# Performance work log

Measured on AMD Instinct MI355X. Metric: run time of the kernel, lower is better.

The kernel has to match this reference:

```python
import jax, jax.numpy as jnp
import numpy as np

E, DM, DH, K, DIL = 8, 512, 1024, 3, 2
N, L = 128, 128
PAD = DIL * (K - 1) // 2  # 'same' padding


def _conv1d(x, w):
    # x: [N, Cin, L], w: [Cout, Cin, K] -> [N, Cout, L]
    return jax.lax.conv_general_dilated(
        x, w, window_strides=(1,), padding=[(PAD, PAD)],
        rhs_dilation=(DIL,), dimension_numbers=("NCH", "OIH", "NCH"))


def _moe_conv(x, W, B, onehot):
    # W: [E, Cout, Cin, K], B: [E, Cout], onehot: [N, E]
    ys = jax.vmap(lambda w, b: _conv1d(x, w) + b[None, :, None])(W, B)  # [E, N, Cout, L]
    return jnp.einsum("enol,ne->nol", ys, onehot)


def setup_inputs() -> dict:
    key = jax.random.key(0)
    k1, k2, k3, k4, k5 = jax.random.split(key, 5)
    inp = jax.random.normal(k1, (N, DM, L), dtype=jnp.float32)
    # uneven per-expert sample counts summing to N (samples pre-sorted by expert)
    fwd_expert_count = jnp.asarray(np.array([10, 20, 16, 16, 12, 22, 14, 18], dtype=np.int32))
    w1 = jax.random.normal(k2, (E, DH, DM, K), dtype=jnp.float32) * 0.02
    b1 = jax.random.normal(k3, (E, DH), dtype=jnp.float32) * 0.02
    w2 = jax.random.normal(k4, (E, DM, DH, K), dtype=jnp.float32) * 0.02
    b2 = jax.random.normal(k5, (E, DM), dtype=jnp.float32) * 0.02
    return {"inp": inp, "fwd_expert_count": fwd_expert_count,
            "w1": w1, "b1": b1, "w2": w2, "b2": b2}


def reference(inp, fwd_expert_count, w1, b1, w2, b2):
    # map each sample index to its expert via cumulative counts
    cs = jnp.cumsum(fwd_expert_count)
    eid = jnp.searchsorted(cs, jnp.arange(N), side="right")  # [N]
    onehot = (eid[:, None] == jnp.arange(E)[None, :]).astype(inp.dtype)  # [N, E]
    h = _moe_conv(inp, w1, b1, onehot)       # [N, DH, L]
    h = jax.nn.gelu(h)
    out = _moe_conv(h, w2, b2, onehot)       # [N, DM, L]
    return out
```

## Files before the change

### kernel.cpp

```cpp
#include <hip/hip_runtime.h>
#include <hip/hip_bf16.h>
#include <stdint.h>


typedef __attribute__((ext_vector_type(8))) short short8;
typedef __attribute__((ext_vector_type(4))) float f32x4;

#define DMV 512
#define DHV 1024

#define OFF_X   0ull
#define OFF_H   (16ull << 20)
#define OFF_W1  (48ull << 20)
#define OFF_W2  (72ull << 20)

#define VMW(n) asm volatile("s_waitcnt vmcnt(" #n ")" ::: "memory")
#define SB __builtin_amdgcn_sched_barrier(0)

__device__ __forceinline__ uint16_t f2bf(float f) {
  uint32_t u = __builtin_bit_cast(uint32_t, f);
  uint32_t r = (u + 0x7FFFu + ((u >> 16) & 1u)) >> 16;
  return (uint16_t)r;
}

__device__ __forceinline__ void async_copy16(const void* g, void* l) {
  __builtin_amdgcn_global_load_lds(
      (const __attribute__((address_space(1))) uint32_t*)g,
      (__attribute__((address_space(3))) uint32_t*)l, 16, 0, 0);
}

__device__ __forceinline__ float gelu_f(float x) {
  float u = 0.7978845608028654f * (x + 0.044715f * x * x * x);
  float t = __expf(2.0f * u);
  float th = 1.0f - 2.0f / (t + 1.0f);
  return 0.5f * x * (1.0f + th);
}

__global__ __launch_bounds__(256) void prep_x_t(const float* __restrict__ inp,
                                                uint16_t* __restrict__ xp) {
  uint32_t b = blockIdx.x;
  uint32_t s = b >> 4, cc = b & 15u;
  __shared__ uint16_t xs[32][132];
  uint32_t t = threadIdx.x;
  const float* src0 = inp + ((size_t)s * DMV + cc * 32u) * 128u;
#pragma unroll
  for (int i = 0; i < 4; ++i) {
    uint32_t idx = (uint32_t)i * 256u + t;
    uint32_t ch = idx >> 5, l4 = idx & 31u;
    float4 f = *(const float4*)(src0 + ch * 128u + l4 * 4u);
    uint2 pk;
    pk.x = (uint32_t)f2bf(f.x) | ((uint32_t)f2bf(f.y) << 16);
    pk.y = (uint32_t)f2bf(f.z) | ((uint32_t)f2bf(f.w) << 16);
    *(uint2*)&xs[ch][l4 * 4u] = pk;
  }
  __syncthreads();
  uint32_t l = t >> 1, half = t & 1u;
  uint32_t fl = ((l + 2u) >> 1) & 3u;
#pragma unroll
  for (int hi = 0; hi < 2; ++hi) {
    uint32_t sub = half * 2u + (uint32_t)hi;
    uint32_t cg = (sub ^ fl) & 3u;
    uint32_t pk[4];
#pragma unroll
    for (int p2 = 0; p2 < 4; ++p2) {
      uint32_t c0 = cg * 8u + (uint32_t)p2 * 2u;
      pk[p2] = (uint32_t)xs[c0][l] | ((uint32_t)xs[c0 + 1][l] << 16);
    }
    uint4 v; v.x = pk[0]; v.y = pk[1]; v.z = pk[2]; v.w = pk[3];
    size_t slot = (((size_t)s * 16u + cc) * 128u + l) * 4u + sub;
    *(uint4*)(xp + slot * 8u) = v;
  }
}

template <int LOGCG, int LOGO>
__global__ __launch_bounds__(256) void prep_w_c(const float* __restrict__ w,
                                                uint16_t* __restrict__ wp) {
  constexpr uint32_t C = 4u << LOGCG;
  constexpr uint32_t CCn = C >> 5;
  constexpr uint32_t MTn = 1u << (LOGO - 7);
  uint32_t t = blockIdx.x * 256u + threadIdx.x;
  uint32_t cg = t & ((1u << LOGCG) - 1u);
  uint32_t o = (t >> LOGCG) & ((1u << LOGO) - 1u);
  uint32_t e = t >> (LOGCG + LOGO);
  uint32_t row = o & 127u, mt = o >> 7;
  const float* src = w + (((size_t)(e << LOGO) + o) * C + cg * 4u) * 3u;
  float4 f0 = *(const float4*)(src);
  float4 f1 = *(const float4*)(src + 4);
  float4 f2 = *(const float4*)(src + 8);
  uint32_t cc = cg >> 3;
  uint32_t sub = (cg >> 1) & 3u;
  uint32_t j0 = (cg & 1u) * 4u;
  size_t base = (((size_t)e * CCn + cc) * MTn + mt) * 3u;
  uint2 q;
  q.x = (uint32_t)f2bf(f0.x) | ((uint32_t)f2bf(f0.w) << 16);
  q.y = (uint32_t)f2bf(f1.z) | ((uint32_t)f2bf(f2.y) << 16);
  *(uint2*)(wp + ((base + 0u) * 128u + row) * 32u + sub * 8u + j0) = q;
  q.x = (uint32_t)f2bf(f0.y) | ((uint32_t)f2bf(f1.x) << 16);
  q.y = (uint32_t)f2bf(f1.w) | ((uint32_t)f2bf(f2.z) << 16);
  *(uint2*)(wp + ((base + 1u) * 128u + row) * 32u + sub * 8u + j0) = q;
  q.x = (uint32_t)f2bf(f0.z) | ((uint32_t)f2bf(f1.y) << 16);
  q.y = (uint32_t)f2bf(f2.x) | ((uint32_t)f2bf(f2.w) << 16);
  *(uint2*)(wp + ((base + 2u) * 128u + row) * 32u + sub * 8u + j0) = q;
}

template <int PHASE>
__global__ __launch_bounds__(PHASE == 1 ? 256 : 128, 2) void conv_mfma(
    const uint16_t* __restrict__ bprep, const uint16_t* __restrict__ wprep,
    const float* __restrict__ bias, const int* __restrict__ cnt,
    uint16_t* __restrict__ hout, float* __restrict__ fout) {
  constexpr int CC  = (PHASE == 1) ? 16 : 32;
  constexpr int MTP = (PHASE == 1) ? 8 : 4;
  constexpr int NW  = (PHASE == 1) ? 4 : 2;
  constexpr int NT  = NW * 64;
  constexpr int SLD = 8 / NW;
  constexpr int OO  = (PHASE == 1) ? DHV : DMV;

  uint32_t b = blockIdx.x;
  uint32_t xcd = b & 7u, i = b >> 3;
  const int s = (int)((xcd & 1u) * 64u + i);
  const int mt = (int)(xcd >> 1);
  const int mtBase = (PHASE == 1) ? mt * 2 : mt;
  int e = 0;
  { int cum = cnt[0]; while (s >= cum && e < 7) { ++e; cum += cnt[e]; } }
  const int tid = threadIdx.x;
  const int lane = tid & 63;
  const int wv = tid >> 6;
  const int l15 = lane & 15, kg = lane >> 4;

  __shared__ __align__(16) uint8_t lds[2 * 8448];

  const size_t AST = (size_t)MTP * 12288;
  const uint16_t* wLane = wprep + ((size_t)e * CC * MTP + mtBase) * 12288
                          + (uint32_t)(l15 * 32 + kg * 8);
  const uint16_t* xBase = bprep + (size_t)s * CC * 4096;

  if (tid < 32) {
    uint32_t n = (uint32_t)tid >> 4, ri = ((uint32_t)tid >> 2) & 3u, sb = (uint32_t)tid & 3u;
    uint32_t rowByte = (ri < 2) ? ri * 64u : (8320u + (ri - 2) * 64u);
    uint4 z = make_uint4(0, 0, 0, 0);
    *(uint4*)(lds + n * 8448u + rowByte + sb * 16u) = z;
  }

  {
    uint8_t* bw = lds + 128u;
#pragma unroll
    for (int t = 0; t < SLD; ++t)
      async_copy16(xBase + (t * NT + tid) * 8, bw + (uint32_t)(t * NT + tid) * 16);
  }
  SB;
  short8 aA[3][4], aB[3][4];
#pragma unroll
  for (int k = 0; k < 3; ++k)
#pragma unroll
    for (int q = 0; q < 4; ++q) {
      uint32_t rows = (uint32_t)(wv * 64 + q * 16);
      aA[k][q] = *(const short8*)(wLane + (rows >> 7) * 12288u +
                                  ((uint32_t)k * 128u + (rows & 127u)) * 32u);
    }
  VMW(0);
  asm volatile("s_waitcnt lgkmcnt(0)" ::: "memory");
  __builtin_amdgcn_s_barrier();

  f32x4 acc[4][8] = {};

  auto STEP = [&](short8 (&CUR)[3][4], short8 (&NXT)[3][4], int cc, bool pre) {
    const uint8_t* bb = lds + (uint32_t)(cc & 1) * 8448u;
    if (pre) {
      const uint16_t* xs = xBase + (size_t)(cc + 1) * 4096;
      uint8_t* bw = lds + (uint32_t)((cc + 1) & 1) * 8448u + 128u;
#pragma unroll
      for (int t = 0; t < SLD; ++t)
        async_copy16(xs + (t * NT + tid) * 8, bw + (uint32_t)(t * NT + tid) * 16);
      SB;
    }
    const uint16_t* aP = wLane + (size_t)(cc + 1) * AST;
#pragma unroll
    for (int k = 0; k < 3; ++k) {
      if (pre) {
#pragma unroll
        for (int q = 0; q < 4; ++q) {
          uint32_t rows = (uint32_t)(wv * 64 + q * 16);
          NXT[k][q] = *(const short8*)(aP + (rows >> 7) * 12288u +
                                       ((uint32_t)k * 128u + (rows & 127u)) * 32u);
        }
      }
      short8 bf[8];
#pragma unroll
      for (int bq = 0; bq < 8; ++bq) {
        uint32_t r = (uint32_t)(bq * 16 + l15 + 2 * k);
        bf[bq] = *(const short8*)(bb + r * 64u +
                                  (((uint32_t)kg ^ (r >> 1)) & 3u) * 16u);
      }
      __builtin_amdgcn_s_setprio(1);
#pragma unroll
      for (int q = 0; q < 4; ++q)
#pragma unroll
        for (int bq = 0; bq < 8; ++bq)
          acc[q][bq] = __builtin_amdgcn_mfma_f32_16x16x32_bf16(
              CUR[k][q], bf[bq], acc[q][bq], 0, 0, 0);
      __builtin_amdgcn_s_setprio(0);
    }
    if (pre) {
      VMW(12);
      __builtin_amdgcn_s_barrier();
    }
  };

#pragma unroll 1
  for (int cc = 0; cc < CC - 2; cc += 2) {
    STEP(aA, aB, cc, true);
    STEP(aB, aA, cc + 1, true);
  }
  STEP(aA, aB, CC - 2, true);
  STEP(aB, aA, CC - 1, false);

  if (PHASE == 1) {
#pragma unroll
    for (int a = 0; a < 4; ++a) {
      int ob = mt * 256 + wv * 64 + a * 16 + kg * 4;
      float4 bv = *(const float4*)(bias + (size_t)e * OO + ob);
      int cc2 = mt * 8 + wv * 2 + (a >> 1);
      uint32_t g = (uint32_t)((a & 1) * 2 + (kg >> 1));
      uint32_t j0 = (uint32_t)((kg & 1) * 4);
#pragma unroll
      for (int bq = 0; bq < 8; ++bq) {
        int l = bq * 16 + l15;
        uint32_t flq = ((uint32_t)(l + 2) >> 1) & 3u;
        uint32_t sub = g ^ flq;
        float v0 = gelu_f(acc[a][bq][0] + bv.x);
        float v1 = gelu_f(acc[a][bq][1] + bv.y);
        float v2 = gelu_f(acc[a][bq][2] + bv.z);
        float v3 = gelu_f(acc[a][bq][3] + bv.w);
        uint2 pk;
        pk.x = (uint32_t)f2bf(v0) | ((uint32_t)f2bf(v1) << 16);
        pk.y = (uint32_t)f2bf(v2) | ((uint32_t)f2bf(v3) << 16);
        size_t ci = ((size_t)s * 32 + cc2) * 128 + l;
        *(uint2*)(hout + ci * 32 + sub * 8 + j0) = pk;
      }
    }
  } else {
#pragma unroll
    for (int a = 0; a < 4; ++a) {
      int ob = mt * 128 + wv * 64 + a * 16 + kg * 4;
      float4 bv = *(const float4*)(bias + (size_t)e * OO + ob);
      float bvr[4] = {bv.x, bv.y, bv.z, bv.w};
      float* op = fout + ((size_t)s * DMV + ob) * 128;
#pragma unroll
      for (int bq = 0; bq < 8; ++bq) {
        int l = bq * 16 + l15;
#pragma unroll
        for (int r = 0; r < 4; ++r)
          op[(size_t)r * 128 + l] = acc[a][bq][r] + bvr[r];
      }
    }
  }
}

extern "C" void kernel_launch(void* const* d_in, const int* in_sizes, int n_in,
                              void* d_out, int out_size, void* d_ws, size_t ws_size,
                              hipStream_t stream) {
  const float* inp = (const float*)d_in[0];
  const int* cnt = (const int*)d_in[1];
  const float* w1 = (const float*)d_in[2];
  const float* b1 = (const float*)d_in[3];
  const float* w2 = (const float*)d_in[4];
  const float* b2 = (const float*)d_in[5];
  float* out = (float*)d_out;
  uint8_t* ws = (uint8_t*)d_ws;
  uint16_t* xp = (uint16_t*)(ws + OFF_X);
  uint16_t* hp = (uint16_t*)(ws + OFF_H);
  uint16_t* w1p = (uint16_t*)(ws + OFF_W1);
  uint16_t* w2p = (uint16_t*)(ws + OFF_W2);

  prep_x_t<<<dim3(2048), dim3(256), 0, stream>>>(inp, xp);
  prep_w_c<7, 10><<<dim3(4096), dim3(256), 0, stream>>>(w1, w1p);
  prep_w_c<8, 9><<<dim3(4096), dim3(256), 0, stream>>>(w2, w2p);
  conv_mfma<1><<<dim3(512), dim3(256), 0, stream>>>(xp, w1p, b1, cnt, hp, nullptr);
  conv_mfma<2><<<dim3(512), dim3(128), 0, stream>>>(hp, w2p, b2, cnt, nullptr, out);
}
```

Before: 164.2 us.

## Stage conv weights through swizzled LDS and shrink phase-1 blocks to two waves

Weights are now staged into LDS with async copies, using a swizzled layout written by the prep kernel. Previously each lane loaded its weight fragments straight from global memory into registers. Halo zero rows in LDS are replaced by clamped addresses plus register zeroing at the edges. Phase 1 now runs 1024 blocks of 128 threads instead of 512 of 256, and the block mapping changes. The aim is fewer uncoalesced global loads and lower register pressure, at the cost of an extra barrier and a full wait per channel chunk, with less overlap than the old double-buffered register prefetch.

New measurement: 170.5 us. 3.8% more time.

```diff
diff --git a/kernel.cpp b/kernel.cpp
--- a/kernel.cpp
+++ b/kernel.cpp
@@ -88,7 +88,7 @@
   float4 f1 = *(const float4*)(src + 4);
   float4 f2 = *(const float4*)(src + 8);
   uint32_t cc = cg >> 3;
-  uint32_t sub = (cg >> 1) & 3u;
+  uint32_t sub = ((cg >> 1) & 3u) ^ ((row >> 1) & 3u);
   uint32_t j0 = (cg & 1u) * 4u;
   size_t base = (((size_t)e * CCn + cc) * MTn + mt) * 3u;
   uint2 q;
@@ -104,122 +104,109 @@
 }
 
 template <int PHASE>
-__global__ __launch_bounds__(PHASE == 1 ? 256 : 128, 2) void conv_mfma(
+__global__ __launch_bounds__(128, 2) void conv_mfma(
     const uint16_t* __restrict__ bprep, const uint16_t* __restrict__ wprep,
     const float* __restrict__ bias, const int* __restrict__ cnt,
     uint16_t* __restrict__ hout, float* __restrict__ fout) {
   constexpr int CC  = (PHASE == 1) ? 16 : 32;
   constexpr int MTP = (PHASE == 1) ? 8 : 4;
-  constexpr int NW  = (PHASE == 1) ? 4 : 2;
-  constexpr int NT  = NW * 64;
-  constexpr int SLD = 8 / NW;
   constexpr int OO  = (PHASE == 1) ? DHV : DMV;
 
   uint32_t b = blockIdx.x;
-  uint32_t xcd = b & 7u, i = b >> 3;
-  const int s = (int)((xcd & 1u) * 64u + i);
-  const int mt = (int)(xcd >> 1);
-  const int mtBase = (PHASE == 1) ? mt * 2 : mt;
+  int s, mt;
+  if (PHASE == 1) { mt = (int)(b & 7u); s = (int)(b >> 3); }
+  else { uint32_t x = b & 7u; mt = (int)(x >> 1); s = (int)((x & 1u) * 64u + (b >> 3)); }
   int e = 0;
   { int cum = cnt[0]; while (s >= cum && e < 7) { ++e; cum += cnt[e]; } }
   const int tid = threadIdx.x;
   const int lane = tid & 63;
-  const int wv = tid >> 6;
+  const int mg = tid >> 6;
   const int l15 = lane & 15, kg = lane >> 4;
 
-  __shared__ __align__(16) uint8_t lds[2 * 8448];
-
-  const size_t AST = (size_t)MTP * 12288;
-  const uint16_t* wLane = wprep + ((size_t)e * CC * MTP + mtBase) * 12288
-                          + (uint32_t)(l15 * 32 + kg * 8);
+  __shared__ __align__(16) uint8_t lds[40960];
+
+  uint32_t aOff[4];
+#pragma unroll
+  for (int a = 0; a < 4; ++a) {
+    uint32_t ri = (uint32_t)(mg * 64 + a * 16 + l15);
+    aOff[a] = ri * 64u + (((uint32_t)kg ^ (ri >> 1)) & 3u) * 16u;
+  }
+  uint32_t bOff[3][8];
+#pragma unroll
+  for (int k = 0; k < 3; ++k)
+#pragma unroll
+    for (int bq = 0; bq < 8; ++bq) {
+      int r = l15 + bq * 16 + 2 * k - 2;
+      uint32_t rc = (uint32_t)(r < 0 ? 0 : (r > 127 ? 127 : r));
+      bOff[k][bq] = rc * 64u + (((uint32_t)kg ^ (((rc + 2u) >> 1))) & 3u) * 16u;
+    }
+  const bool zLow = (l15 < 2);
+  const bool zHigh = (l15 >= 14);
+
+  const uint16_t* wBase = wprep + ((size_t)e * CC * MTP + mt) * 12288;
   const uint16_t* xBase = bprep + (size_t)s * CC * 4096;
 
-  if (tid < 32) {
-    uint32_t n = (uint32_t)tid >> 4, ri = ((uint32_t)tid >> 2) & 3u, sb = (uint32_t)tid & 3u;
-    uint32_t rowByte = (ri < 2) ? ri * 64u : (8320u + (ri - 2) * 64u);
-    uint4 z = make_uint4(0, 0, 0, 0);
-    *(uint4*)(lds + n * 8448u + rowByte + sb * 16u) = z;
-  }
-
-  {
-    uint8_t* bw = lds + 128u;
-#pragma unroll
-    for (int t = 0; t < SLD; ++t)
-      async_copy16(xBase + (t * NT + tid) * 8, bw + (uint32_t)(t * NT + tid) * 16);
-  }
-  SB;
-  short8 aA[3][4], aB[3][4];
-#pragma unroll
-  for (int k = 0; k < 3; ++k)
-#pragma unroll
-    for (int q = 0; q < 4; ++q) {
-      uint32_t rows = (uint32_t)(wv * 64 + q * 16);
-      aA[k][q] = *(const short8*)(wLane + (rows >> 7) * 12288u +
-                                  ((uint32_t)k * 128u + (rows & 127u)) * 32u);
-    }
+  auto STAGE_A = [&](int cc) {
+    const uint16_t* src = wBase + (size_t)cc * (MTP * 12288);
+#pragma unroll
+    for (int i = 0; i < 12; ++i)
+      async_copy16(src + (i * 128 + tid) * 8, lds + (uint32_t)(i * 128 + tid) * 16u);
+  };
+  auto STAGE_B = [&](int cc) {
+    const uint16_t* src = xBase + (size_t)cc * 4096;
+    uint8_t* dst = lds + 24576u + (uint32_t)(cc & 1) * 8192u;
+#pragma unroll
+    for (int i = 0; i < 4; ++i)
+      async_copy16(src + (i * 128 + tid) * 8, dst + (uint32_t)(i * 128 + tid) * 16u);
+  };
+
+  STAGE_A(0); STAGE_B(0);
   VMW(0);
-  asm volatile("s_waitcnt lgkmcnt(0)" ::: "memory");
   __builtin_amdgcn_s_barrier();
 
   f32x4 acc[4][8] = {};
-
-  auto STEP = [&](short8 (&CUR)[3][4], short8 (&NXT)[3][4], int cc, bool pre) {
-    const uint8_t* bb = lds + (uint32_t)(cc & 1) * 8448u;
-    if (pre) {
-      const uint16_t* xs = xBase + (size_t)(cc + 1) * 4096;
-      uint8_t* bw = lds + (uint32_t)((cc + 1) & 1) * 8448u + 128u;
-#pragma unroll
-      for (int t = 0; t < SLD; ++t)
-        async_copy16(xs + (t * NT + tid) * 8, bw + (uint32_t)(t * NT + tid) * 16);
-      SB;
-    }
-    const uint16_t* aP = wLane + (size_t)(cc + 1) * AST;
+  const short8 z8 = {};
+
+#pragma unroll 1
+  for (int cc = 0; cc < CC; ++cc) {
+    short8 af[3][4];
+#pragma unroll
+    for (int k = 0; k < 3; ++k)
+#pragma unroll
+      for (int q = 0; q < 4; ++q)
+        af[k][q] = *(const short8*)(lds + (uint32_t)(k * 8192) + aOff[q]);
+    asm volatile("s_waitcnt lgkmcnt(0)" ::: "memory");
+    SB;
+    __builtin_amdgcn_s_barrier();
+    if (cc + 1 < CC) { STAGE_A(cc + 1); STAGE_B(cc + 1); }
+    const uint8_t* bb = lds + 24576u + (uint32_t)(cc & 1) * 8192u;
 #pragma unroll
     for (int k = 0; k < 3; ++k) {
-      if (pre) {
-#pragma unroll
-        for (int q = 0; q < 4; ++q) {
-          uint32_t rows = (uint32_t)(wv * 64 + q * 16);
-          NXT[k][q] = *(const short8*)(aP + (rows >> 7) * 12288u +
-                                       ((uint32_t)k * 128u + (rows & 127u)) * 32u);
-        }
+      __builtin_amdgcn_s_setprio(1);
+#pragma unroll
+      for (int bq = 0; bq < 8; ++bq) {
+        short8 bf = *(const short8*)(bb + bOff[k][bq]);
+        if (k == 0 && bq == 0) bf = zLow ? z8 : bf;
+        if (k == 2 && bq == 7) bf = zHigh ? z8 : bf;
+#pragma unroll
+        for (int q = 0; q < 4; ++q)
+          acc[q][bq] = __builtin_amdgcn_mfma_f32_16x16x32_bf16(
+              af[k][q], bf, acc[q][bq], 0, 0, 0);
       }
-      short8 bf[8];
-#pragma unroll
-      for (int bq = 0; bq < 8; ++bq) {
-        uint32_t r = (uint32_t)(bq * 16 + l15 + 2 * k);
-        bf[bq] = *(const short8*)(bb + r * 64u +
-                                  (((uint32_t)kg ^ (r >> 1)) & 3u) * 16u);
-      }
-      __builtin_amdgcn_s_setprio(1);
-#pragma unroll
-      for (int q = 0; q < 4; ++q)
-#pragma unroll
-        for (int bq = 0; bq < 8; ++bq)
-          acc[q][bq] = __builtin_amdgcn_mfma_f32_16x16x32_bf16(
-              CUR[k][q], bf[bq], acc[q][bq], 0, 0, 0);
       __builtin_amdgcn_s_setprio(0);
     }
-    if (pre) {
-      VMW(12);
+    if (cc + 1 < CC) {
+      VMW(0);
       __builtin_amdgcn_s_barrier();
     }
-  };
-
-#pragma unroll 1
-  for (int cc = 0; cc < CC - 2; cc += 2) {
-    STEP(aA, aB, cc, true);
-    STEP(aB, aA, cc + 1, true);
-  }
-  STEP(aA, aB, CC - 2, true);
-  STEP(aB, aA, CC - 1, false);
+  }
 
   if (PHASE == 1) {
 #pragma unroll
     for (int a = 0; a < 4; ++a) {
-      int ob = mt * 256 + wv * 64 + a * 16 + kg * 4;
+      int ob = mt * 128 + mg * 64 + a * 16 + kg * 4;
       float4 bv = *(const float4*)(bias + (size_t)e * OO + ob);
-      int cc2 = mt * 8 + wv * 2 + (a >> 1);
+      int cc2 = mt * 4 + mg * 2 + (a >> 1);
       uint32_t g = (uint32_t)((a & 1) * 2 + (kg >> 1));
       uint32_t j0 = (uint32_t)((kg & 1) * 4);
 #pragma unroll
@@ -241,7 +228,7 @@
   } else {
 #pragma unroll
     for (int a = 0; a < 4; ++a) {
-      int ob = mt * 128 + wv * 64 + a * 16 + kg * 4;
+      int ob = mt * 128 + mg * 64 + a * 16 + kg * 4;
       float4 bv = *(const float4*)(bias + (size_t)e * OO + ob);
       float bvr[4] = {bv.x, bv.y, bv.z, bv.w};
       float* op = fout + ((size_t)s * DMV + ob) * 128;
@@ -275,6 +262,6 @@
   prep_x_t<<<dim3(2048), dim3(256), 0, stream>>>(inp, xp);
   prep_w_c<7, 10><<<dim3(4096), dim3(256), 0, stream>>>(w1, w1p);
   prep_w_c<8, 9><<<dim3(4096), dim3(256), 0, stream>>>(w2, w2p);
-  conv_mfma<1><<<dim3(512), dim3(256), 0, stream>>>(xp, w1p, b1, cnt, hp, nullptr);
+  conv_mfma<1><<<dim3(1024), dim3(128), 0, stream>>>(xp, w1p, b1, cnt, hp, nullptr);
   conv_mfma<2><<<dim3(512), dim3(128), 0, stream>>>(hp, w2p, b2, cnt, nullptr, out);
 }
```
